# Kernel optimization log

Measured on AMD Instinct MI355X. Metric: run time of the kernel, lower is better.

The kernel has to match this reference:

```python
import jax, jax.numpy as jnp
import numpy as np

EMBED = 256; M = 8; DV = 32; L = 4; K = 4; SCALE = 0.5
LEVELS = [(128, 128), (64, 64), (32, 32), (16, 16)]  # (H_l, W_l), static
S_TOTAL = sum(h * w for h, w in LEVELS)  # 21760


def _linear_params(key, fan_in, fan_out):
    kw, kb = jax.random.split(key)
    lim = 1.0 / np.sqrt(fan_in)
    W = jax.random.uniform(kw, (fan_in, fan_out), minval=-lim, maxval=lim, dtype=jnp.float32)
    b = jax.random.uniform(kb, (fan_out,), minval=-lim, maxval=lim, dtype=jnp.float32)
    return W, b


def setup_inputs() -> dict:
    key = jax.random.key(0)
    ks = jax.random.split(key, 8)
    N, Q = 2, 8192
    W_off, b_off = _linear_params(ks[0], EMBED, M * L * K * 2)
    W_attn, b_attn = _linear_params(ks[1], EMBED, M * L * K)
    W_val, b_val = _linear_params(ks[2], EMBED, M * DV)
    W_out, b_out = _linear_params(ks[3], M * DV, EMBED)
    queries = jax.random.normal(ks[4], (N, Q, EMBED), dtype=jnp.float32)
    query_geometry_logits = jax.random.normal(ks[5], (N, Q, 4), dtype=jnp.float32)
    value = jax.random.normal(ks[6], (N, S_TOTAL, EMBED), dtype=jnp.float32)
    value_mask = jnp.ones((N, S_TOTAL, 1), dtype=jnp.float32)
    return {"queries": queries, "query_geometry_logits": query_geometry_logits,
            "value": value, "value_mask": value_mask,
            "W_off": W_off, "b_off": b_off, "W_attn": W_attn, "b_attn": b_attn,
            "W_val": W_val, "b_val": b_val, "W_out": W_out, "b_out": b_out}


def _bilinear(img_flat, grid, H, W):
    """grid_sample(mode=bilinear, padding=zeros, align_corners=False).
    img_flat: (B, H*W, C); grid: (B, P, 2) with (x, y) in [-1, 1]."""
    x = (grid[..., 0] + 1.0) * (W * 0.5) - 0.5
    y = (grid[..., 1] + 1.0) * (H * 0.5) - 0.5
    x0f, y0f = jnp.floor(x), jnp.floor(y)
    wx, wy = x - x0f, y - y0f
    x0, y0 = x0f.astype(jnp.int32), y0f.astype(jnp.int32)

    def gather(xi, yi, w):
        valid = (xi >= 0) & (xi < W) & (yi >= 0) & (yi < H)
        idx = jnp.clip(yi, 0, H - 1) * W + jnp.clip(xi, 0, W - 1)
        v = jnp.take_along_axis(img_flat, idx[..., None], axis=1)
        return v * (w * valid)[..., None]

    return (gather(x0, y0, (1 - wx) * (1 - wy)) + gather(x0 + 1, y0, wx * (1 - wy))
            + gather(x0, y0 + 1, (1 - wx) * wy) + gather(x0 + 1, y0 + 1, wx * wy))


def _forward(queries, query_geometry_logits, value, value_mask,
             W_off, b_off, W_attn, b_attn, W_val, b_val, W_out, b_out):
    N, Q, _ = queries.shape
    # attention weights: (N, Q, M, L*K), softmax over the L*K sampling points
    attn = jax.nn.softmax((queries @ W_attn + b_attn).reshape(N, Q, M, L * K), axis=-1)
    # sampling offsets: (N, Q, M, L*K, 2)
    deltas = (queries @ W_off + b_off).reshape(N, Q, M, L * K, 2)
    # reference boxes: sigmoid -> (cx, cy, w, h) in [0, 1]
    b_q = jax.nn.sigmoid(query_geometry_logits)
    xy, wh = b_q[..., :2], b_q[..., 2:]
    scale = wh * (1.0 / K) * SCALE                       # (N, Q, 2)
    pos = xy[:, :, None, None, :] + deltas * scale[:, :, None, None, :]  # (N,Q,M,LK,2)
    # value projection + mask
    v_masked = value_mask * (value @ W_val + b_val)      # (N, S, M*DV)
    # collapse (N, M) for per-head grid sampling
    grid = jnp.clip(2.0 * pos.transpose(0, 2, 1, 3, 4).reshape(N * M, Q, L * K, 2) - 1.0, -1.0, 1.0)
    outs, start = [], 0
    for li, (H, W) in enumerate(LEVELS):
        v_l = v_masked[:, start:start + H * W, :].reshape(N, H * W, M, DV)
        v_l = v_l.transpose(0, 2, 1, 3).reshape(N * M, H * W, DV)
        g_l = grid[:, :, K * li:K * (li + 1), :].reshape(N * M, Q * K, 2)
        s_l = _bilinear(v_l, g_l, H, W)                  # (N*M, Q*K, DV)
        outs.append(s_l.reshape(N, M, Q, K, DV))
        start += H * W
    vals = jnp.concatenate(outs, axis=3)                 # (N, M, Q, L*K, DV)
    vals = vals.transpose(0, 2, 1, 3, 4)                 # (N, Q, M, L*K, DV)
    out = jnp.sum(attn[..., None] * vals, axis=3).reshape(N, Q, M * DV)
    return out @ W_out + b_out                           # (N, Q, EMBED)


def reference(queries, query_geometry_logits, value, value_mask,
              W_off, b_off, W_attn, b_attn, W_val, b_val, W_out, b_out):
    return _forward(queries, query_geometry_logits, value, value_mask,
                    W_off, b_off, W_attn, b_attn, W_val, b_val, W_out, b_out)
```

## Files before the change

kernel.cpp:

```cpp
#include <hip/hip_runtime.h>
#include <math.h>

#define EMBED   256
#define M_HEADS 8
#define DVAL    32
#define LK      16
#define S_TOTAL 21760
#define NQ      8192
#define NROWS   (2 * NQ)
#define QBS     16

typedef __attribute__((ext_vector_type(8))) short s16x8;
typedef __attribute__((ext_vector_type(4))) float f32x4;
typedef unsigned short u16;
typedef unsigned int   u32;

__device__ __forceinline__ short f2bf(float f) {
    unsigned u = __float_as_uint(f);
    u += 0x7fffu + ((u >> 16) & 1u);
    return (short)(u >> 16);
}
__device__ __forceinline__ float bf2f(short h) {
    return __uint_as_float(((unsigned)(u16)h) << 16);
}

#define V_OFF     0
#define V_FLTS    5570560
#define PA_OFF    (V_OFF + V_FLTS)
#define PA_FLTS   6291456
#define MID_OFF   (PA_OFF + PA_FLTS)
#define MID_FLTS  2097152
#define WHI_OFF   (MID_OFF + MID_FLTS)
#define WOA_FLTS  49152
#define WLO_OFF   (WHI_OFF + WOA_FLTS)
#define WV_OFF    (WLO_OFF + WOA_FLTS)
#define WO_OFF    (WV_OFF + 32768)

__global__ __launch_bounds__(256) void prep_kernel(
    const float* __restrict__ W_off, const float* __restrict__ W_attn,
    u16* __restrict__ Whi,           u16* __restrict__ Wlo,
    const float* __restrict__ W_val, u16* __restrict__ Wv,
    const float* __restrict__ W_out, u16* __restrict__ Wo)
{
    const int b = blockIdx.x;
    const int t = threadIdx.x;

    if (b < 512) {
        const int flat = b * 256 + t;
        const int which = flat >> 16;
        const int e = flat & 65535;
        const int k = e >> 8, c = e & 255;
        const float f = which ? W_out[k * 256 + c] : W_val[k * 256 + c];
        const int kt = k >> 5, qd = (k >> 3) & 3, j = k & 7;
        const int idx = (((kt * 256 + c) << 2) + qd) * 8 + j;
        (which ? Wo : Wv)[idx] = (u16)f2bf(f);
    } else {
        const int flat = (b - 512) * 256 + t;
        const int k = flat / 384, c = flat - k * 384;
        const float f = (c < 256) ? W_off[k * 256 + c] : W_attn[k * 128 + (c - 256)];
        const short h = f2bf(f);
        const short lo = f2bf(f - bf2f(h));
        const int kt = k >> 5, qd = (k >> 3) & 3, j = k & 7;
        const int idx = (((kt * 384 + c) << 2) + qd) * 8 + j;
        Whi[idx] = (u16)h;
        Wlo[idx] = (u16)lo;
    }
}

__global__ __launch_bounds__(256, 2) void vproj_kernel(
    const float* __restrict__ value,
    const float* __restrict__ vmask,
    const u16* __restrict__ Wpk,
    const float* __restrict__ b_val,
    u16* __restrict__ v_out)
{
    const int t  = threadIdx.x;
    const int w  = t >> 6, l = t & 63;
    const int c  = l & 15, qd = l >> 4;
    const int c0 = w * 64;

    s16x8 B[8][4];
    #pragma unroll
    for (int kt = 0; kt < 8; ++kt)
        #pragma unroll
        for (int nt = 0; nt < 4; ++nt)
            B[kt][nt] = *(const s16x8*)(Wpk + (((kt * 256 + c0 + nt * 16 + c) << 2) + qd) * 8);

    float bias[4];
    #pragma unroll
    for (int nt = 0; nt < 4; ++nt) bias[nt] = b_val[c0 + nt * 16 + c];

    #pragma unroll
    for (int tt = 0; tt < 2; ++tt) {
        const int tile = blockIdx.x + tt * 1360;
        const int r0 = tile * 16;
        const float* __restrict__ ap = value + (size_t)(r0 + c) * EMBED + qd * 8;

        float4 a0[8], a1[8];
        #pragma unroll
        for (int kt = 0; kt < 8; ++kt) {
            a0[kt] = *(const float4*)(ap + kt * 32);
            a1[kt] = *(const float4*)(ap + kt * 32 + 4);
        }

        f32x4 acc[4] = {};
        #pragma unroll
        for (int kt = 0; kt < 8; ++kt) {
            const s16x8 a = (s16x8){ f2bf(a0[kt].x), f2bf(a0[kt].y), f2bf(a0[kt].z), f2bf(a0[kt].w),
                                     f2bf(a1[kt].x), f2bf(a1[kt].y), f2bf(a1[kt].z), f2bf(a1[kt].w) };
            #pragma unroll
            for (int nt = 0; nt < 4; ++nt)
                acc[nt] = __builtin_amdgcn_mfma_f32_16x16x32_bf16(a, B[kt][nt], acc[nt], 0, 0, 0);
        }

        #pragma unroll
        for (int r = 0; r < 4; ++r) {
            const int grow = r0 + qd * 4 + r;
            const int n = (grow >= S_TOTAL) ? 1 : 0;
            const int s = grow - n * S_TOTAL;
            const float mk = vmask[grow];
            #pragma unroll
            for (int nt = 0; nt < 4; ++nt) {
                const int col = c0 + nt * 16 + c;
                const int hm = col >> 5, d = col & 31;
                v_out[((size_t)(n * M_HEADS + hm) * S_TOTAL + s) * DVAL + d] =
                    (u16)f2bf((acc[nt][r] + bias[nt]) * mk);
            }
        }
    }
}

__global__ __launch_bounds__(256) void qproj_kernel(
    const float* __restrict__ queries,
    const float* __restrict__ qgl,
    const u16* __restrict__ Whi, const u16* __restrict__ Wlo,
    const float* __restrict__ b_off, const float* __restrict__ b_attn,
    float* __restrict__ pa)
{
    __shared__ float s_off[16][260];
    __shared__ float s_attn[16][132];
    __shared__ float s_geom[16][4];

    const int t  = threadIdx.x;
    const int w  = t >> 6, l = t & 63;
    const int c  = l & 15, qd = l >> 4;
    const int row0 = blockIdx.x * 16;
    const int c0 = w * 96;

    if (t < 16) {
        const float* g = &qgl[(size_t)(row0 + t) * 4];
        s_geom[t][0] = 1.f / (1.f + __expf(-g[0]));
        s_geom[t][1] = 1.f / (1.f + __expf(-g[1]));
        s_geom[t][2] = (1.f / (1.f + __expf(-g[2]))) * 0.125f;
        s_geom[t][3] = (1.f / (1.f + __expf(-g[3]))) * 0.125f;
    }

    f32x4 acc[6] = {};

    for (int kt = 0; kt < 8; ++kt) {
        s16x8 ah, al, bh[6], bl[6];
        {
            const float* qp = queries + (size_t)(row0 + c) * EMBED + kt * 32 + qd * 8;
            const float4 v0 = *(const float4*)qp;
            const float4 v1 = *(const float4*)(qp + 4);
            const short h0 = f2bf(v0.x), h1 = f2bf(v0.y), h2 = f2bf(v0.z), h3 = f2bf(v0.w);
            const short h4 = f2bf(v1.x), h5 = f2bf(v1.y), h6 = f2bf(v1.z), h7 = f2bf(v1.w);
            ah = (s16x8){ h0, h1, h2, h3, h4, h5, h6, h7 };
            al = (s16x8){ f2bf(v0.x - bf2f(h0)), f2bf(v0.y - bf2f(h1)),
                          f2bf(v0.z - bf2f(h2)), f2bf(v0.w - bf2f(h3)),
                          f2bf(v1.x - bf2f(h4)), f2bf(v1.y - bf2f(h5)),
                          f2bf(v1.z - bf2f(h6)), f2bf(v1.w - bf2f(h7)) };
        }
        #pragma unroll
        for (int nt = 0; nt < 6; ++nt) {
            const int idx = (((kt * 384 + c0 + nt * 16 + c) << 2) + qd) * 8;
            bh[nt] = *(const s16x8*)(Whi + idx);
            bl[nt] = *(const s16x8*)(Wlo + idx);
        }
        #pragma unroll
        for (int nt = 0; nt < 6; ++nt) {
            acc[nt] = __builtin_amdgcn_mfma_f32_16x16x32_bf16(ah, bh[nt], acc[nt], 0, 0, 0);
            acc[nt] = __builtin_amdgcn_mfma_f32_16x16x32_bf16(ah, bl[nt], acc[nt], 0, 0, 0);
            acc[nt] = __builtin_amdgcn_mfma_f32_16x16x32_bf16(al, bh[nt], acc[nt], 0, 0, 0);
        }
    }

    #pragma unroll
    for (int nt = 0; nt < 6; ++nt) {
        const int col = c0 + nt * 16 + c;
        #pragma unroll
        for (int r = 0; r < 4; ++r) {
            const int row = qd * 4 + r;
            if (col < 256) s_off[row][col] = acc[nt][r] + b_off[col];
            else           s_attn[row][col - 256] = acc[nt][r] + b_attn[col - 256];
        }
    }
    __syncthreads();

    if (t < 128) {
        const int qi = t >> 3, hm = t & 7;
        float* a = &s_attn[qi][hm * LK];
        float mx = a[0];
        #pragma unroll
        for (int i = 1; i < LK; ++i) mx = fmaxf(mx, a[i]);
        float s = 0.f;
        #pragma unroll
        for (int i = 0; i < LK; ++i) { const float e = __expf(a[i] - mx); a[i] = e; s += e; }
        const float inv = 1.f / s;
        #pragma unroll
        for (int i = 0; i < LK; ++i) a[i] *= inv;
    }
    __syncthreads();

    for (int p = t; p < 16 * 128; p += 256) {
        const int qi = p >> 7;
        const int pt = p & 127;
        const int lvl = (pt & 15) >> 2;
        const float Wl = (float)(128 >> lvl);
        const float px = fmaf(s_off[qi][2 * pt + 0], s_geom[qi][2], s_geom[qi][0]);
        const float py = fmaf(s_off[qi][2 * pt + 1], s_geom[qi][3], s_geom[qi][1]);
        const float gx = fminf(fmaxf(2.f * px - 1.f, -1.f), 1.f);
        const float gy = fminf(fmaxf(2.f * py - 1.f, -1.f), 1.f);
        const float x = (gx + 1.f) * (Wl * 0.5f) - 0.5f;
        const float y = (gy + 1.f) * (Wl * 0.5f) - 0.5f;
        const size_t idx = ((size_t)(row0 + qi) * 128 + pt) * 3;
        pa[idx + 0] = x;
        pa[idx + 1] = y;
        pa[idx + 2] = s_attn[qi][pt];
    }
}

__global__ __launch_bounds__(256) void sample_kernel(
    const float* __restrict__ pa,
    const u16* __restrict__ v_tab,
    u16* __restrict__ mid)
{
    __shared__ int4   s_idx[QBS * 17];
    __shared__ float4 s_w[QBS * 17];

    const int t    = threadIdx.x;
    const int m    = blockIdx.x & 7;
    const int rest = blockIdx.x >> 3;
    const int qc   = rest & 511;
    const int n    = rest >> 9;
    const int q0   = qc * QBS;

    {
        const int qi = t >> 4, lk = t & 15;
        const int lvl   = lk >> 2;
        const int Wl    = 128 >> lvl;
        const int start = (lvl == 0) ? 0 : (lvl == 1) ? 16384 : (lvl == 2) ? 20480 : 21504;

        const size_t prow = ((size_t)(n * NQ + q0 + qi)) * 128 + m * 16 + lk;
        const float x  = pa[prow * 3 + 0];
        const float y  = pa[prow * 3 + 1];
        const float aw = pa[prow * 3 + 2];

        const float x0f = floorf(x), y0f = floorf(y);
        const int   x0 = (int)x0f, y0 = (int)y0f;
        const float wx = x - x0f, wy = y - y0f;

        const float vx0 = (x0 >= 0) ? 1.f : 0.f;
        const float vx1 = (x0 + 1 <= Wl - 1) ? 1.f : 0.f;
        const float vy0 = (y0 >= 0) ? 1.f : 0.f;
        const float vy1 = (y0 + 1 <= Wl - 1) ? 1.f : 0.f;

        const int xc0 = max(x0, 0);
        const int xc1 = min(x0 + 1, Wl - 1);
        const int yc0 = max(y0, 0);
        const int yc1 = min(y0 + 1, Wl - 1);

        const int e = qi * 17 + lk;
        s_idx[e] = make_int4((start + yc0 * Wl + xc0) * DVAL,
                             (start + yc0 * Wl + xc1) * DVAL,
                             (start + yc1 * Wl + xc0) * DVAL,
                             (start + yc1 * Wl + xc1) * DVAL);
        s_w[e] = make_float4(aw * (1.f - wx) * (1.f - wy) * vx0 * vy0,
                             aw * wx * (1.f - wy) * vx1 * vy0,
                             aw * (1.f - wx) * wy * vx0 * vy1,
                             aw * wx * wy * vx1 * vy1);
    }
    __syncthreads();

    const int g = t >> 4, dp = t & 15;
    const u16* __restrict__ vbp =
        v_tab + (size_t)(n * M_HEADS + m) * S_TOTAL * DVAL + 2 * dp;

    float acc0 = 0.f, acc1 = 0.f;
    #pragma unroll
    for (int lk = 0; lk < LK; ++lk) {
        const int4   id = s_idx[g * 17 + lk];
        const float4 w  = s_w[g * 17 + lk];
        const u32 u0 = *(const u32*)(vbp + id.x);
        const u32 u1 = *(const u32*)(vbp + id.y);
        const u32 u2 = *(const u32*)(vbp + id.z);
        const u32 u3 = *(const u32*)(vbp + id.w);
        acc0 = fmaf(w.x, __uint_as_float(u0 << 16), acc0);
        acc1 = fmaf(w.x, __uint_as_float(u0 & 0xffff0000u), acc1);
        acc0 = fmaf(w.y, __uint_as_float(u1 << 16), acc0);
        acc1 = fmaf(w.y, __uint_as_float(u1 & 0xffff0000u), acc1);
        acc0 = fmaf(w.z, __uint_as_float(u2 << 16), acc0);
        acc1 = fmaf(w.z, __uint_as_float(u2 & 0xffff0000u), acc1);
        acc0 = fmaf(w.w, __uint_as_float(u3 << 16), acc0);
        acc1 = fmaf(w.w, __uint_as_float(u3 & 0xffff0000u), acc1);
    }

    const u32 packed = ((u32)(u16)f2bf(acc1) << 16) | (u32)(u16)f2bf(acc0);
    *(u32*)(mid + ((size_t)(n * NQ + q0 + g)) * EMBED + m * DVAL + 2 * dp) = packed;
}

__global__ __launch_bounds__(256, 2) void out_kernel(
    const u16* __restrict__ mid,
    const u16* __restrict__ Wpk,
    const float* __restrict__ b_out,
    float* __restrict__ out)
{
    const int t  = threadIdx.x;
    const int w  = t >> 6, l = t & 63;
    const int c  = l & 15, qd = l >> 4;
    const int c0 = w * 64;

    s16x8 B[8][4];
    #pragma unroll
    for (int kt = 0; kt < 8; ++kt)
        #pragma unroll
        for (int nt = 0; nt < 4; ++nt)
            B[kt][nt] = *(const s16x8*)(Wpk + (((kt * 256 + c0 + nt * 16 + c) << 2) + qd) * 8);

    float bias[4];
    #pragma unroll
    for (int nt = 0; nt < 4; ++nt) bias[nt] = b_out[c0 + nt * 16 + c];

    for (int tile = blockIdx.x; tile < 1024; tile += 512) {
        const int r0 = tile * 16;
        const u16* __restrict__ ap = mid + (size_t)(r0 + c) * EMBED + qd * 8;

        s16x8 a[8];
        #pragma unroll
        for (int kt = 0; kt < 8; ++kt)
            a[kt] = *(const s16x8*)(ap + kt * 32);

        f32x4 acc[4] = {};
        #pragma unroll
        for (int kt = 0; kt < 8; ++kt)
            #pragma unroll
            for (int nt = 0; nt < 4; ++nt)
                acc[nt] = __builtin_amdgcn_mfma_f32_16x16x32_bf16(a[kt], B[kt][nt], acc[nt], 0, 0, 0);

        #pragma unroll
        for (int r = 0; r < 4; ++r) {
            const int row = r0 + qd * 4 + r;
            #pragma unroll
            for (int nt = 0; nt < 4; ++nt)
                out[(size_t)row * EMBED + c0 + nt * 16 + c] = acc[nt][r] + bias[nt];
        }
    }
}

extern "C" void kernel_launch(void* const* d_in, const int* in_sizes, int n_in,
                              void* d_out, int out_size, void* d_ws, size_t ws_size,
                              hipStream_t stream) {
    (void)in_sizes; (void)n_in; (void)out_size; (void)ws_size;

    const float* queries = (const float*)d_in[0];
    const float* qgl     = (const float*)d_in[1];
    const float* value   = (const float*)d_in[2];
    const float* vmask   = (const float*)d_in[3];
    const float* W_off   = (const float*)d_in[4];
    const float* b_off   = (const float*)d_in[5];
    const float* W_attn  = (const float*)d_in[6];
    const float* b_attn  = (const float*)d_in[7];
    const float* W_val   = (const float*)d_in[8];
    const float* b_val   = (const float*)d_in[9];
    const float* W_out   = (const float*)d_in[10];
    const float* b_out   = (const float*)d_in[11];

    float* ws   = (float*)d_ws;
    u16*  v_ws  = (u16*)(ws + V_OFF);
    float* pa   = ws + PA_OFF;
    u16*  mid   = (u16*)(ws + MID_OFF);
    u16*  whi   = (u16*)(ws + WHI_OFF);
    u16*  wlo   = (u16*)(ws + WLO_OFF);
    u16*  wvpk  = (u16*)(ws + WV_OFF);
    u16*  wopk  = (u16*)(ws + WO_OFF);
    float* outp = (float*)d_out;

    prep_kernel<<<896, 256, 0, stream>>>(W_off, W_attn, whi, wlo,
                                         W_val, wvpk, W_out, wopk);

    vproj_kernel<<<1360, 256, 0, stream>>>(value, vmask, wvpk, b_val, v_ws);
    qproj_kernel<<<NROWS / 16, 256, 0, stream>>>(queries, qgl, whi, wlo,
                                                 b_off, b_attn, pa);
    sample_kernel<<<2 * (NQ / QBS) * M_HEADS, 256, 0, stream>>>(pa, v_ws, mid);
    out_kernel<<<512, 256, 0, stream>>>(mid, wopk, b_out, outp);
}
```

Measured before the change: 217.7 us.

## Fuse query projection with per-head bilinear sampling and persistent-grid value projection

Merges the query projection (offsets plus attention logits) into the sampling kernel. Each block now computes only its head's 48 projection columns for 64 queries and keeps the positions and softmax weights in shared memory, so the intermediate position/weight buffer is never written or read back in global memory and one kernel launch disappears. The value projection kernel also switches from a fixed two-tiles-per-block layout to a grid-stride loop over 512 blocks. The cost is that the query rows are re-read and re-converted once per head (8 times), and the sampling phase now runs in four sequential 16-query rounds with extra barriers.

Result: slower. 225.5 us (+3.6%).

```diff
diff --git a/kernel.cpp b/kernel.cpp
--- a/kernel.cpp
+++ b/kernel.cpp
@@ -8,7 +8,6 @@
 #define S_TOTAL 21760
 #define NQ      8192
 #define NROWS   (2 * NQ)
-#define QBS     16
 
 typedef __attribute__((ext_vector_type(8))) short s16x8;
 typedef __attribute__((ext_vector_type(4))) float f32x4;
@@ -90,9 +89,7 @@
     #pragma unroll
     for (int nt = 0; nt < 4; ++nt) bias[nt] = b_val[c0 + nt * 16 + c];
 
-    #pragma unroll
-    for (int tt = 0; tt < 2; ++tt) {
-        const int tile = blockIdx.x + tt * 1360;
+    for (int tile = blockIdx.x; tile < 2720; tile += 512) {
         const int r0 = tile * 16;
         const float* __restrict__ ap = value + (size_t)(r0 + c) * EMBED + qd * 8;
 
@@ -130,76 +127,89 @@
     }
 }
 
-__global__ __launch_bounds__(256) void qproj_kernel(
+__global__ __launch_bounds__(256) void qsamp_kernel(
     const float* __restrict__ queries,
     const float* __restrict__ qgl,
     const u16* __restrict__ Whi, const u16* __restrict__ Wlo,
     const float* __restrict__ b_off, const float* __restrict__ b_attn,
-    float* __restrict__ pa)
+    const u16* __restrict__ v_tab,
+    u16* __restrict__ mid)
 {
-    __shared__ float s_off[16][260];
-    __shared__ float s_attn[16][132];
-    __shared__ float s_geom[16][4];
-
-    const int t  = threadIdx.x;
-    const int w  = t >> 6, l = t & 63;
-    const int c  = l & 15, qd = l >> 4;
-    const int row0 = blockIdx.x * 16;
-    const int c0 = w * 96;
-
-    if (t < 16) {
-        const float* g = &qgl[(size_t)(row0 + t) * 4];
+    __shared__ float  s_offm[64][33];
+    __shared__ float  s_attnm[64][17];
+    __shared__ float  s_geom[64][4];
+    __shared__ int4   s_idx[16 * 17];
+    __shared__ float4 s_w[16 * 17];
+
+    const int t    = threadIdx.x;
+    const int m    = blockIdx.x & 7;
+    const int rest = blockIdx.x >> 3;
+    const int qc   = rest & 127;
+    const int n    = rest >> 7;
+    const int q0   = qc * 64;
+    const int rowbase = n * NQ + q0;
+
+    const int w = t >> 6, l = t & 63;
+    const int c = l & 15, qd = l >> 4;
+    const int row0 = rowbase + w * 16;
+    const int ct0 = 32 * m, ct1 = 32 * m + 16, ct2 = 256 + 16 * m;
+
+    f32x4 acc0 = {}, acc1 = {}, acc2 = {};
+
+    for (int kt = 0; kt < 8; ++kt) {
+        const float* qp = queries + (size_t)(row0 + c) * EMBED + kt * 32 + qd * 8;
+        const float4 v0 = *(const float4*)qp;
+        const float4 v1 = *(const float4*)(qp + 4);
+        const short h0 = f2bf(v0.x), h1 = f2bf(v0.y), h2 = f2bf(v0.z), h3 = f2bf(v0.w);
+        const short h4 = f2bf(v1.x), h5 = f2bf(v1.y), h6 = f2bf(v1.z), h7 = f2bf(v1.w);
+        const s16x8 ah = (s16x8){ h0, h1, h2, h3, h4, h5, h6, h7 };
+        const s16x8 al = (s16x8){ f2bf(v0.x - bf2f(h0)), f2bf(v0.y - bf2f(h1)),
+                                  f2bf(v0.z - bf2f(h2)), f2bf(v0.w - bf2f(h3)),
+                                  f2bf(v1.x - bf2f(h4)), f2bf(v1.y - bf2f(h5)),
+                                  f2bf(v1.z - bf2f(h6)), f2bf(v1.w - bf2f(h7)) };
+
+        const int i0 = (((kt * 384 + ct0 + c) << 2) + qd) * 8;
+        const int i1 = (((kt * 384 + ct1 + c) << 2) + qd) * 8;
+        const int i2 = (((kt * 384 + ct2 + c) << 2) + qd) * 8;
+        const s16x8 bh0 = *(const s16x8*)(Whi + i0), bl0 = *(const s16x8*)(Wlo + i0);
+        const s16x8 bh1 = *(const s16x8*)(Whi + i1), bl1 = *(const s16x8*)(Wlo + i1);
+        const s16x8 bh2 = *(const s16x8*)(Whi + i2), bl2 = *(const s16x8*)(Wlo + i2);
+
+        acc0 = __builtin_amdgcn_mfma_f32_16x16x32_bf16(ah, bh0, acc0, 0, 0, 0);
+        acc0 = __builtin_amdgcn_mfma_f32_16x16x32_bf16(ah, bl0, acc0, 0, 0, 0);
+        acc0 = __builtin_amdgcn_mfma_f32_16x16x32_bf16(al, bh0, acc0, 0, 0, 0);
+        acc1 = __builtin_amdgcn_mfma_f32_16x16x32_bf16(ah, bh1, acc1, 0, 0, 0);
+        acc1 = __builtin_amdgcn_mfma_f32_16x16x32_bf16(ah, bl1, acc1, 0, 0, 0);
+        acc1 = __builtin_amdgcn_mfma_f32_16x16x32_bf16(al, bh1, acc1, 0, 0, 0);
+        acc2 = __builtin_amdgcn_mfma_f32_16x16x32_bf16(ah, bh2, acc2, 0, 0, 0);
+        acc2 = __builtin_amdgcn_mfma_f32_16x16x32_bf16(ah, bl2, acc2, 0, 0, 0);
+        acc2 = __builtin_amdgcn_mfma_f32_16x16x32_bf16(al, bh2, acc2, 0, 0, 0);
+    }
+
+    {
+        const float bo0 = b_off[ct0 + c];
+        const float bo1 = b_off[ct1 + c];
+        const float ba  = b_attn[16 * m + c];
+        #pragma unroll
+        for (int r = 0; r < 4; ++r) {
+            const int row = w * 16 + qd * 4 + r;
+            s_offm[row][c]      = acc0[r] + bo0;
+            s_offm[row][16 + c] = acc1[r] + bo1;
+            s_attnm[row][c]     = acc2[r] + ba;
+        }
+    }
+
+    if (t < 64) {
+        const float* g = &qgl[(size_t)(rowbase + t) * 4];
         s_geom[t][0] = 1.f / (1.f + __expf(-g[0]));
         s_geom[t][1] = 1.f / (1.f + __expf(-g[1]));
         s_geom[t][2] = (1.f / (1.f + __expf(-g[2]))) * 0.125f;
         s_geom[t][3] = (1.f / (1.f + __expf(-g[3]))) * 0.125f;
     }
-
-    f32x4 acc[6] = {};
-
-    for (int kt = 0; kt < 8; ++kt) {
-        s16x8 ah, al, bh[6], bl[6];
-        {
-            const float* qp = queries + (size_t)(row0 + c) * EMBED + kt * 32 + qd * 8;
-            const float4 v0 = *(const float4*)qp;
-            const float4 v1 = *(const float4*)(qp + 4);
-            const short h0 = f2bf(v0.x), h1 = f2bf(v0.y), h2 = f2bf(v0.z), h3 = f2bf(v0.w);
-            const short h4 = f2bf(v1.x), h5 = f2bf(v1.y), h6 = f2bf(v1.z), h7 = f2bf(v1.w);
-            ah = (s16x8){ h0, h1, h2, h3, h4, h5, h6, h7 };
-            al = (s16x8){ f2bf(v0.x - bf2f(h0)), f2bf(v0.y - bf2f(h1)),
-                          f2bf(v0.z - bf2f(h2)), f2bf(v0.w - bf2f(h3)),
-                          f2bf(v1.x - bf2f(h4)), f2bf(v1.y - bf2f(h5)),
-                          f2bf(v1.z - bf2f(h6)), f2bf(v1.w - bf2f(h7)) };
-        }
-        #pragma unroll
-        for (int nt = 0; nt < 6; ++nt) {
-            const int idx = (((kt * 384 + c0 + nt * 16 + c) << 2) + qd) * 8;
-            bh[nt] = *(const s16x8*)(Whi + idx);
-            bl[nt] = *(const s16x8*)(Wlo + idx);
-        }
-        #pragma unroll
-        for (int nt = 0; nt < 6; ++nt) {
-            acc[nt] = __builtin_amdgcn_mfma_f32_16x16x32_bf16(ah, bh[nt], acc[nt], 0, 0, 0);
-            acc[nt] = __builtin_amdgcn_mfma_f32_16x16x32_bf16(ah, bl[nt], acc[nt], 0, 0, 0);
-            acc[nt] = __builtin_amdgcn_mfma_f32_16x16x32_bf16(al, bh[nt], acc[nt], 0, 0, 0);
-        }
-    }
-
-    #pragma unroll
-    for (int nt = 0; nt < 6; ++nt) {
-        const int col = c0 + nt * 16 + c;
-        #pragma unroll
-        for (int r = 0; r < 4; ++r) {
-            const int row = qd * 4 + r;
-            if (col < 256) s_off[row][col] = acc[nt][r] + b_off[col];
-            else           s_attn[row][col - 256] = acc[nt][r] + b_attn[col - 256];
-        }
-    }
     __syncthreads();
 
-    if (t < 128) {
-        const int qi = t >> 3, hm = t & 7;
-        float* a = &s_attn[qi][hm * LK];
+    if (t < 64) {
+        float* a = s_attnm[t];
         float mx = a[0];
         #pragma unroll
         for (int i = 1; i < LK; ++i) mx = fmaxf(mx, a[i]);
@@ -212,101 +222,77 @@
     }
     __syncthreads();
 
-    for (int p = t; p < 16 * 128; p += 256) {
-        const int qi = p >> 7;
-        const int pt = p & 127;
-        const int lvl = (pt & 15) >> 2;
-        const float Wl = (float)(128 >> lvl);
-        const float px = fmaf(s_off[qi][2 * pt + 0], s_geom[qi][2], s_geom[qi][0]);
-        const float py = fmaf(s_off[qi][2 * pt + 1], s_geom[qi][3], s_geom[qi][1]);
-        const float gx = fminf(fmaxf(2.f * px - 1.f, -1.f), 1.f);
-        const float gy = fminf(fmaxf(2.f * py - 1.f, -1.f), 1.f);
-        const float x = (gx + 1.f) * (Wl * 0.5f) - 0.5f;
-        const float y = (gy + 1.f) * (Wl * 0.5f) - 0.5f;
-        const size_t idx = ((size_t)(row0 + qi) * 128 + pt) * 3;
-        pa[idx + 0] = x;
-        pa[idx + 1] = y;
-        pa[idx + 2] = s_attn[qi][pt];
-    }
-}
-
-__global__ __launch_bounds__(256) void sample_kernel(
-    const float* __restrict__ pa,
-    const u16* __restrict__ v_tab,
-    u16* __restrict__ mid)
-{
-    __shared__ int4   s_idx[QBS * 17];
-    __shared__ float4 s_w[QBS * 17];
-
-    const int t    = threadIdx.x;
-    const int m    = blockIdx.x & 7;
-    const int rest = blockIdx.x >> 3;
-    const int qc   = rest & 511;
-    const int n    = rest >> 9;
-    const int q0   = qc * QBS;
-
-    {
-        const int qi = t >> 4, lk = t & 15;
-        const int lvl   = lk >> 2;
-        const int Wl    = 128 >> lvl;
-        const int start = (lvl == 0) ? 0 : (lvl == 1) ? 16384 : (lvl == 2) ? 20480 : 21504;
-
-        const size_t prow = ((size_t)(n * NQ + q0 + qi)) * 128 + m * 16 + lk;
-        const float x  = pa[prow * 3 + 0];
-        const float y  = pa[prow * 3 + 1];
-        const float aw = pa[prow * 3 + 2];
-
-        const float x0f = floorf(x), y0f = floorf(y);
-        const int   x0 = (int)x0f, y0 = (int)y0f;
-        const float wx = x - x0f, wy = y - y0f;
-
-        const float vx0 = (x0 >= 0) ? 1.f : 0.f;
-        const float vx1 = (x0 + 1 <= Wl - 1) ? 1.f : 0.f;
-        const float vy0 = (y0 >= 0) ? 1.f : 0.f;
-        const float vy1 = (y0 + 1 <= Wl - 1) ? 1.f : 0.f;
-
-        const int xc0 = max(x0, 0);
-        const int xc1 = min(x0 + 1, Wl - 1);
-        const int yc0 = max(y0, 0);
-        const int yc1 = min(y0 + 1, Wl - 1);
-
-        const int e = qi * 17 + lk;
-        s_idx[e] = make_int4((start + yc0 * Wl + xc0) * DVAL,
-                             (start + yc0 * Wl + xc1) * DVAL,
-                             (start + yc1 * Wl + xc0) * DVAL,
-                             (start + yc1 * Wl + xc1) * DVAL);
-        s_w[e] = make_float4(aw * (1.f - wx) * (1.f - wy) * vx0 * vy0,
-                             aw * wx * (1.f - wy) * vx1 * vy0,
-                             aw * (1.f - wx) * wy * vx0 * vy1,
-                             aw * wx * wy * vx1 * vy1);
-    }
-    __syncthreads();
-
-    const int g = t >> 4, dp = t & 15;
+    const int g  = t >> 4, dp = t & 15;
     const u16* __restrict__ vbp =
         v_tab + (size_t)(n * M_HEADS + m) * S_TOTAL * DVAL + 2 * dp;
 
-    float acc0 = 0.f, acc1 = 0.f;
-    #pragma unroll
-    for (int lk = 0; lk < LK; ++lk) {
-        const int4   id = s_idx[g * 17 + lk];
-        const float4 w  = s_w[g * 17 + lk];
-        const u32 u0 = *(const u32*)(vbp + id.x);
-        const u32 u1 = *(const u32*)(vbp + id.y);
-        const u32 u2 = *(const u32*)(vbp + id.z);
-        const u32 u3 = *(const u32*)(vbp + id.w);
-        acc0 = fmaf(w.x, __uint_as_float(u0 << 16), acc0);
-        acc1 = fmaf(w.x, __uint_as_float(u0 & 0xffff0000u), acc1);
-        acc0 = fmaf(w.y, __uint_as_float(u1 << 16), acc0);
-        acc1 = fmaf(w.y, __uint_as_float(u1 & 0xffff0000u), acc1);
-        acc0 = fmaf(w.z, __uint_as_float(u2 << 16), acc0);
-        acc1 = fmaf(w.z, __uint_as_float(u2 & 0xffff0000u), acc1);
-        acc0 = fmaf(w.w, __uint_as_float(u3 << 16), acc0);
-        acc1 = fmaf(w.w, __uint_as_float(u3 & 0xffff0000u), acc1);
-    }
-
-    const u32 packed = ((u32)(u16)f2bf(acc1) << 16) | (u32)(u16)f2bf(acc0);
-    *(u32*)(mid + ((size_t)(n * NQ + q0 + g)) * EMBED + m * DVAL + 2 * dp) = packed;
+    for (int rd = 0; rd < 4; ++rd) {
+        const int qb = rd * 16;
+        {
+            const int qi  = qb + (t >> 4);
+            const int lk  = t & 15;
+            const int lvl = lk >> 2;
+            const int Wl  = 128 >> lvl;
+            const int start = (lvl == 0) ? 0 : (lvl == 1) ? 16384 : (lvl == 2) ? 20480 : 21504;
+            const float Wlf = (float)Wl;
+
+            const float px = fmaf(s_offm[qi][2 * lk + 0], s_geom[qi][2], s_geom[qi][0]);
+            const float py = fmaf(s_offm[qi][2 * lk + 1], s_geom[qi][3], s_geom[qi][1]);
+            const float gx = fminf(fmaxf(2.f * px - 1.f, -1.f), 1.f);
+            const float gy = fminf(fmaxf(2.f * py - 1.f, -1.f), 1.f);
+            const float x  = (gx + 1.f) * (Wlf * 0.5f) - 0.5f;
+            const float y  = (gy + 1.f) * (Wlf * 0.5f) - 0.5f;
+            const float aw = s_attnm[qi][lk];
+
+            const float x0f = floorf(x), y0f = floorf(y);
+            const int   x0 = (int)x0f, y0 = (int)y0f;
+            const float wx = x - x0f, wy = y - y0f;
+
+            const float vx0 = (x0 >= 0) ? 1.f : 0.f;
+            const float vx1 = (x0 + 1 <= Wl - 1) ? 1.f : 0.f;
+            const float vy0 = (y0 >= 0) ? 1.f : 0.f;
+            const float vy1 = (y0 + 1 <= Wl - 1) ? 1.f : 0.f;
+
+            const int xc0 = max(x0, 0);
+            const int xc1 = min(x0 + 1, Wl - 1);
+            const int yc0 = max(y0, 0);
+            const int yc1 = min(y0 + 1, Wl - 1);
+
+            const int e = (t >> 4) * 17 + lk;
+            s_idx[e] = make_int4((start + yc0 * Wl + xc0) * DVAL,
+                                 (start + yc0 * Wl + xc1) * DVAL,
+                                 (start + yc1 * Wl + xc0) * DVAL,
+                                 (start + yc1 * Wl + xc1) * DVAL);
+            s_w[e] = make_float4(aw * (1.f - wx) * (1.f - wy) * vx0 * vy0,
+                                 aw * wx * (1.f - wy) * vx1 * vy0,
+                                 aw * (1.f - wx) * wy * vx0 * vy1,
+                                 aw * wx * wy * vx1 * vy1);
+        }
+        __syncthreads();
+
+        float a0 = 0.f, a1 = 0.f;
+        #pragma unroll
+        for (int lk = 0; lk < LK; ++lk) {
+            const int4   id = s_idx[g * 17 + lk];
+            const float4 ww = s_w[g * 17 + lk];
+            const u32 u0 = *(const u32*)(vbp + id.x);
+            const u32 u1 = *(const u32*)(vbp + id.y);
+            const u32 u2 = *(const u32*)(vbp + id.z);
+            const u32 u3 = *(const u32*)(vbp + id.w);
+            a0 = fmaf(ww.x, __uint_as_float(u0 << 16), a0);
+            a1 = fmaf(ww.x, __uint_as_float(u0 & 0xffff0000u), a1);
+            a0 = fmaf(ww.y, __uint_as_float(u1 << 16), a0);
+            a1 = fmaf(ww.y, __uint_as_float(u1 & 0xffff0000u), a1);
+            a0 = fmaf(ww.z, __uint_as_float(u2 << 16), a0);
+            a1 = fmaf(ww.z, __uint_as_float(u2 & 0xffff0000u), a1);
+            a0 = fmaf(ww.w, __uint_as_float(u3 << 16), a0);
+            a1 = fmaf(ww.w, __uint_as_float(u3 & 0xffff0000u), a1);
+        }
+
+        const u32 packed = ((u32)(u16)f2bf(a1) << 16) | (u32)(u16)f2bf(a0);
+        *(u32*)(mid + ((size_t)(rowbase + qb + g)) * EMBED + m * DVAL + 2 * dp) = packed;
+        __syncthreads();
+    }
 }
 
 __global__ __launch_bounds__(256, 2) void out_kernel(
@@ -377,7 +363,6 @@
 
     float* ws   = (float*)d_ws;
     u16*  v_ws  = (u16*)(ws + V_OFF);
-    float* pa   = ws + PA_OFF;
     u16*  mid   = (u16*)(ws + MID_OFF);
     u16*  whi   = (u16*)(ws + WHI_OFF);
     u16*  wlo   = (u16*)(ws + WLO_OFF);
@@ -388,9 +373,8 @@
     prep_kernel<<<896, 256, 0, stream>>>(W_off, W_attn, whi, wlo,
                                          W_val, wvpk, W_out, wopk);
 
-    vproj_kernel<<<1360, 256, 0, stream>>>(value, vmask, wvpk, b_val, v_ws);
-    qproj_kernel<<<NROWS / 16, 256, 0, stream>>>(queries, qgl, whi, wlo,
-                                                 b_off, b_attn, pa);
-    sample_kernel<<<2 * (NQ / QBS) * M_HEADS, 256, 0, stream>>>(pa, v_ws, mid);
+    vproj_kernel<<<512, 256, 0, stream>>>(value, vmask, wvpk, b_val, v_ws);
+    qsamp_kernel<<<2 * 128 * M_HEADS, 256, 0, stream>>>(queries, qgl, whi, wlo,
+                                                        b_off, b_attn, v_ws, mid);
     out_kernel<<<512, 256, 0, stream>>>(mid, wopk, b_out, outp);
 }
```
